# Kernel tuning notes

Measured on AMD Instinct MI355X. Metric: run time of the kernel, lower is better.

The kernel has to match this reference:

```python
import jax, jax.numpy as jnp
import numpy as np
import math

B, S, HID = 1, 2048, 4096
NH, NKV, HD = 32, 8, 128
N_REP = NH // NKV
ROPE_THETA = 10000.0


def setup_inputs() -> dict:
    key = jax.random.key(0)
    ks = jax.random.split(key, 5)
    hidden_states = jax.random.normal(ks[0], (B, S, HID), dtype=jnp.float32)
    # additive causal mask: 0 on/below diagonal, -1e9 above
    causal = jnp.triu(jnp.full((S, S), -1e9, dtype=jnp.float32), k=1)
    attention_mask = causal[None, None, :, :]
    wq = jax.random.normal(ks[1], (HID, NH * HD), dtype=jnp.float32) * 0.02
    wk = jax.random.normal(ks[2], (HID, NKV * HD), dtype=jnp.float32) * 0.02
    wv = jax.random.normal(ks[3], (HID, NKV * HD), dtype=jnp.float32) * 0.02
    wo = jax.random.normal(ks[4], (NH * HD, HID), dtype=jnp.float32) * 0.02
    return {"hidden_states": hidden_states, "attention_mask": attention_mask,
            "wq": wq, "wk": wk, "wv": wv, "wo": wo}


def _rope_cos_sin(seq_len, head_dim, base, dtype):
    inv_freq = 1.0 / (base ** (jnp.arange(0, head_dim, 2, dtype=jnp.float32) / head_dim))
    t = jnp.arange(seq_len, dtype=jnp.float32)
    freqs = jnp.outer(t, inv_freq)          # [S, HD/2]
    emb = jnp.concatenate([freqs, freqs], axis=-1)  # [S, HD]
    return jnp.cos(emb).astype(dtype), jnp.sin(emb).astype(dtype)


def _rotate_interleaved(x):
    # pairs (x0,x1) -> (-x1, x0), interleaved (matches torch stack/reshape trick)
    xp = x.reshape(*x.shape[:-1], -1, 2)
    return jnp.stack([-xp[..., 1], xp[..., 0]], axis=-1).reshape(x.shape)


def reference(hidden_states, attention_mask, wq, wk, wv, wo):
    b, s, _ = hidden_states.shape
    q = (hidden_states @ wq).reshape(b, s, NH, HD).transpose(0, 2, 1, 3)   # [B,NH,S,HD]
    k = (hidden_states @ wk).reshape(b, s, NKV, HD).transpose(0, 2, 1, 3)  # [B,NKV,S,HD]
    v = (hidden_states @ wv).reshape(b, s, NKV, HD).transpose(0, 2, 1, 3)

    cos, sin = _rope_cos_sin(s, HD, ROPE_THETA, hidden_states.dtype)
    cos = cos[None, None, :, :]  # broadcast over batch and heads
    sin = sin[None, None, :, :]
    q = q * cos + _rotate_interleaved(q) * sin
    k = k * cos + _rotate_interleaved(k) * sin

    # repeat_kv: [B,NKV,S,HD] -> [B,NH,S,HD]
    k = jnp.repeat(k, N_REP, axis=1)
    v = jnp.repeat(v, N_REP, axis=1)

    scores = jnp.einsum('bhqd,bhkd->bhqk', q, k) / math.sqrt(HD)
    scores = scores + attention_mask
    attn = jax.nn.softmax(scores.astype(jnp.float32), axis=-1).astype(q.dtype)
    out = jnp.einsum('bhqk,bhkd->bhqd', attn, v)          # [B,NH,S,HD]
    out = out.transpose(0, 2, 1, 3).reshape(b, s, NH * HD)
    return out @ wo
```

## Files before the change

### kernel.cpp

```cpp
#include <hip/hip_runtime.h>

#define S_LEN 2048
#define HID 4096
#define NH 32
#define NKV 8
#define HD 128
#define KVW 1024
#define NQKV 6144

typedef _Float16 f16;
typedef _Float16 f16x8 __attribute__((ext_vector_type(8)));
typedef _Float16 f16x4 __attribute__((ext_vector_type(4)));
typedef float f32x4 __attribute__((ext_vector_type(4)));
typedef float f32x16 __attribute__((ext_vector_type(16)));
typedef unsigned int u32;
typedef u32 u32x4 __attribute__((ext_vector_type(4)));

__device__ __forceinline__ void gll16(const void* g, void* lds) {
  __builtin_amdgcn_global_load_lds((const __attribute__((address_space(1))) void*)g,
                                   (__attribute__((address_space(3))) void*)lds, 16, 0, 0);
}

template<int N> __device__ __forceinline__ void vmwait() {
  if constexpr (N == 0) asm volatile("s_waitcnt vmcnt(0)" ::: "memory");
  else if constexpr (N == 3) asm volatile("s_waitcnt vmcnt(3)" ::: "memory");
  else if constexpr (N == 4) asm volatile("s_waitcnt vmcnt(4)" ::: "memory");
  else static_assert(N == 0 || N == 3 || N == 4, "add vmcnt case");
}

__global__ void k_cast(const float* __restrict__ src, f16* __restrict__ dst) {
  size_t i = ((size_t)blockIdx.x * blockDim.x + threadIdx.x) * 8;
  float4 a = *(const float4*)(src + i);
  float4 b = *(const float4*)(src + i + 4);
  f16x8 o = { (f16)a.x, (f16)a.y, (f16)a.z, (f16)a.w,
              (f16)b.x, (f16)b.y, (f16)b.z, (f16)b.w };
  *(f16x8*)(dst + i) = o;
}

__global__ void k_trig(float4* __restrict__ trig) {
  int id = blockIdx.x * blockDim.x + threadIdx.x;
  int s = id >> 6, i = id & 63;
  int j0 = 2 * i, j1 = 2 * i + 1;
  float f0 = powf(10000.f, -(float)(j0 & 63) / 64.f);
  float f1 = powf(10000.f, -(float)(j1 & 63) / 64.f);
  float a0 = (float)s * f0, a1 = (float)s * f1;
  trig[id] = make_float4(cosf(a0), cosf(a1), sinf(a0), sinf(a1));
}

__global__ void k_transpose(const float* __restrict__ src, f16* __restrict__ dst, int N) {
  __shared__ f16 tile[64][72];
  int nb = blockIdx.x * 64, kb = blockIdx.y * 64;
  int t = threadIdx.x;
  int kl = t >> 4, nc = (t & 15) << 2;
#pragma unroll
  for (int p = 0; p < 4; ++p) {
    int kk = kl + p * 16;
    float4 v = *(const float4*)(src + (size_t)(kb + kk) * N + nb + nc);
    f16x4 h = { (f16)v.x, (f16)v.y, (f16)v.z, (f16)v.w };
    *(f16x4*)(&tile[kk][nc]) = h;
  }
  __syncthreads();
  int nl = t >> 3, c = t & 7;
#pragma unroll
  for (int p = 0; p < 2; ++p) {
    int nn = nl + p * 32;
    f16x8 o;
#pragma unroll
    for (int i = 0; i < 8; ++i) o[i] = tile[c * 8 + i][nn];
    *(f16x8*)(dst + (size_t)(nb + nn) * HID + kb + c * 8) = o;
  }
}

extern __shared__ char smem[];

template<int MODE, int MF, int NF, int WM, int WN>
__global__ __launch_bounds__(WM * WN * 64, 2) void k_gemm4(
    const f16* __restrict__ A, const f16* __restrict__ Bt,
    f16* __restrict__ Qr, f16* __restrict__ Kr, f16* __restrict__ Vt,
    const float4* __restrict__ trig, float* __restrict__ Cout)
{
  constexpr int NTHR = WM * WN * 64;
  constexpr int BM = WM * MF * 16;
  constexpr int BN = WN * NF * 16;
  constexpr int ABYTES = BM * 128;
  constexpr int BBYTES = BN * 128;
  constexpr int RPC = NTHR / 8;
  constexpr int ACALLS = BM / RPC;
  constexpr int BCALLS = BN / RPC;
  constexpr int NT = 64;

  const int tid = threadIdx.x, ln = tid & 63, w = tid >> 6;
  const int la = ln & 15, lg = ln >> 4;
  const int wr = w / WN, wc = w % WN;
  const int m0 = blockIdx.y * BM, n0 = blockIdx.x * BN;

  const char* asrc[ACALLS];
  const char* bsrc[BCALLS];
  int adst[ACALLS > BCALLS ? ACALLS : BCALLS];
#pragma unroll
  for (int c = 0; c < ACALLS; ++c) {
    int r = c * RPC + (tid >> 3);
    int g = (tid & 7) ^ (r & 7);
    asrc[c] = (const char*)A + ((size_t)(m0 + r) * HID + (size_t)g * 8) * 2;
    adst[c] = c * NTHR * 16 + tid * 16;
  }
#pragma unroll
  for (int c = 0; c < BCALLS; ++c) {
    int r = c * RPC + (tid >> 3);
    int g = (tid & 7) ^ (r & 7);
    bsrc[c] = (const char*)Bt + ((size_t)(n0 + r) * HID + (size_t)g * 8) * 2;
  }

  char* const Bbase = smem + 2 * ABYTES;
  f32x4 acc[MF][NF] = {};

#pragma unroll
  for (int c = 0; c < ACALLS; ++c) gll16(asrc[c], smem + adst[c]);
#pragma unroll
  for (int c = 0; c < BCALLS; ++c) gll16(bsrc[c], Bbase + adst[c]);
#pragma unroll
  for (int c = 0; c < BCALLS; ++c) gll16(bsrc[c] + 128, Bbase + BBYTES + adst[c]);
  vmwait<BCALLS>();
  __builtin_amdgcn_s_barrier();

  for (int t = 0; t < NT; ++t) {
    if (t + 1 < NT) {
      char* sa = smem + ((t + 1) & 1) * ABYTES;
#pragma unroll
      for (int c = 0; c < ACALLS; ++c) gll16(asrc[c] + (size_t)(t + 1) * 128, sa + adst[c]);
    }
    if (t + 2 < NT) {
      char* sb = Bbase + ((t + 2) % 3) * BBYTES;
#pragma unroll
      for (int c = 0; c < BCALLS; ++c) gll16(bsrc[c] + (size_t)(t + 2) * 128, sb + adst[c]);
    }
    const char* sa = smem + (t & 1) * ABYTES;
    const char* sb = Bbase + (t % 3) * BBYTES;
#pragma unroll
    for (int ks = 0; ks < 2; ++ks) {
      f16x8 af[MF], bf[NF];
#pragma unroll
      for (int i = 0; i < MF; ++i) {
        int rl = wr * MF * 16 + i * 16 + la;
        af[i] = *(const f16x8*)(sa + rl * 128 + (((ks * 4 + lg) ^ (rl & 7)) * 16));
      }
#pragma unroll
      for (int n = 0; n < NF; ++n) {
        int rb = wc * NF * 16 + n * 16 + la;
        bf[n] = *(const f16x8*)(sb + rb * 128 + (((ks * 4 + lg) ^ (rb & 7)) * 16));
      }
#pragma unroll
      for (int i = 0; i < MF; ++i)
#pragma unroll
        for (int n = 0; n < NF; ++n)
          acc[i][n] = __builtin_amdgcn_mfma_f32_16x16x32_f16(af[i], bf[n], acc[i][n], 0, 0, 0);
    }
    if (t < NT - 2)      vmwait<BCALLS>();
    else if (t == NT - 2) vmwait<0>();
    if (t < NT - 1) __builtin_amdgcn_s_barrier();
  }

#pragma unroll
  for (int mi = 0; mi < MF; ++mi) {
#pragma unroll
    for (int nf = 0; nf < NF; ++nf) {
      f32x4 fr = acc[mi][nf];
      int n = n0 + wc * NF * 16 + nf * 16 + la;
      int mr = m0 + wr * MF * 16 + mi * 16 + lg * 4;
      if (MODE == 0) {
        if (n < HID + KVW) {
          int d = n & 127;
#pragma unroll
          for (int r = 0; r < 4; ++r) {
            float v = fr[r];
            float p = __shfl_xor(v, 1);
            float4 tc = trig[(size_t)(mr + r) * 64 + (d >> 1)];
            float cv = (d & 1) ? tc.y : tc.x;
            float sv = (d & 1) ? tc.w : tc.z;
            float o = v * cv + ((d & 1) ? p : -p) * sv;
            if (n < HID) Qr[(size_t)(mr + r) * HID + n] = (f16)o;
            else         Kr[(size_t)(mr + r) * KVW + (n - HID)] = (f16)o;
          }
        } else {
          int nv = n - (HID + KVW);
          f16x4 o4 = { (f16)fr[0], (f16)fr[1], (f16)fr[2], (f16)fr[3] };
          *(f16x4*)(Vt + (size_t)nv * S_LEN + mr) = o4;
        }
      } else {
#pragma unroll
        for (int r = 0; r < 4; ++r)
          Cout[(size_t)(mr + r) * HID + n] = fr[r];
      }
    }
  }
}

#define KBYTES (64 * 128 * 2)
#define VBYTES (128 * 64 * 2)

__global__ __launch_bounds__(256, 2) void k_attn(
    const f16* __restrict__ Qr, const f16* __restrict__ Kr, const f16* __restrict__ Vt,
    f16* __restrict__ AO)
{
  int bid = blockIdx.x;
  int h, c;
  if (bid < 256) { h = bid >> 3; c = bid & 7; }
  else           { int t = bid - 256; h = t >> 3; c = 15 - (t & 7); }
  const int hkv = h >> 2;
  const int q0c = c * 128;
  const int NT = 2 * c + 2;

  __shared__ char KV[2][KBYTES + VBYTES];

  const int tid = threadIdx.x;
  const int ln = tid & 63, w = tid >> 6;
  const int q = ln & 31;
  const int hi = ln >> 5;
  const int qg = q0c + w * 32 + q;

  size_t ksrc[4], vsrc[4];
  int kdo[4], vdo[4];
#pragma unroll
  for (int j = 0; j < 4; ++j) {
    int kc = w * 4 + j;
    int kr = kc * 4 + (ln >> 4);
    ksrc[j] = ((size_t)kr * KVW + hkv * HD) * 2 + (size_t)(((ln & 15) ^ (kr & 7)) * 16);
    kdo[j] = kc * 1024;
    int vc = w * 4 + j;
    int d = vc * 8 + (ln >> 3);
    vsrc[j] = ((size_t)(hkv * HD + d) * S_LEN) * 2 + (size_t)(((ln & 7) ^ (d & 7)) * 16);
    vdo[j] = KBYTES + vc * 1024;
  }

  f16x8 qf[8];
  {
    const f16* qrow = Qr + (size_t)qg * HID + h * HD + hi * 8;
#pragma unroll
    for (int ks = 0; ks < 8; ++ks) qf[ks] = *(const f16x8*)(qrow + ks * 16);
  }

  f32x16 ot[4] = {};
  float m2 = -3.0e38f, l = 0.f;
  const float K2 = 0.12753256471f;

  int buf = 0;
#pragma unroll
  for (int j = 0; j < 4; ++j) {
    gll16((const char*)Kr + ksrc[j], &KV[0][kdo[j]]);
    gll16((const char*)Vt + vsrc[j], &KV[0][vdo[j]]);
  }

  for (int jt = 0; jt < NT; ++jt) {
    __syncthreads();
    if (jt + 1 < NT) {
      size_t ko = (size_t)(jt + 1) * 64 * KVW * 2;
      size_t vo = (size_t)(jt + 1) * 64 * 2;
#pragma unroll
      for (int j = 0; j < 4; ++j) {
        gll16((const char*)Kr + ksrc[j] + ko, &KV[buf ^ 1][kdo[j]]);
        gll16((const char*)Vt + vsrc[j] + vo, &KV[buf ^ 1][vdo[j]]);
      }
    }
    const int j0 = jt * 64;
    if (j0 <= q0c + w * 32 + 31) {
      const f16* Kb = (const f16*)&KV[buf][0];
      const f16* Vb = (const f16*)&KV[buf][KBYTES];
      f32x16 s0 = {}, s1 = {};
#pragma unroll
      for (int ks = 0; ks < 8; ++ks) {
        int cc = ((ks * 2 + hi) ^ (q & 7)) * 8;
        f16x8 k0 = *(const f16x8*)(Kb + q * 128 + cc);
        f16x8 k1 = *(const f16x8*)(Kb + (q + 32) * 128 + cc);
        s0 = __builtin_amdgcn_mfma_f32_32x32x16_f16(k0, qf[ks], s0, 0, 0, 0);
        s1 = __builtin_amdgcn_mfma_f32_32x32x16_f16(k1, qf[ks], s1, 0, 0, 0);
      }
      const bool nm = (j0 + 63 > q0c + w * 32);
      float p0[16], p1[16];
      float mx = -3.0e38f;
#pragma unroll
      for (int r = 0; r < 16; ++r) {
        float a = s0[r], b = s1[r];
        if (nm) {
          int kvb = j0 + (r & 3) + 8 * (r >> 2) + 4 * hi;
          if (kvb > qg) a = -3.0e38f;
          if (kvb + 32 > qg) b = -3.0e38f;
        }
        p0[r] = a; p1[r] = b;
        mx = fmaxf(mx, fmaxf(a, b));
      }
      mx = fmaxf(mx, __shfl_xor(mx, 32));
      float m2c = mx * K2;
      int defer = (m2c <= m2 + 11.0f);
      if (!__all(defer)) {
        float m2n = fmaxf(m2, m2c);
        float corr = exp2f(m2 - m2n);
        m2 = m2n; l *= corr;
#pragma unroll
        for (int t = 0; t < 4; ++t)
#pragma unroll
          for (int r = 0; r < 16; ++r) ot[t][r] *= corr;
      }
      float sum = 0.f;
#pragma unroll
      for (int r = 0; r < 16; ++r) {
        p0[r] = exp2f(__builtin_fmaf(p0[r], K2, -m2));
        p1[r] = exp2f(__builtin_fmaf(p1[r], K2, -m2));
        sum += p0[r] + p1[r];
      }
      l += sum + __shfl_xor(sum, 32);
      u32 pw0[8], pw1[8];
#pragma unroll
      for (int t = 0; t < 8; ++t) {
        pw0[t] = __builtin_bit_cast(u32, __builtin_amdgcn_cvt_pkrtz(p0[2 * t], p0[2 * t + 1]));
        pw1[t] = __builtin_bit_cast(u32, __builtin_amdgcn_cvt_pkrtz(p1[2 * t], p1[2 * t + 1]));
      }
      f16x8 pf[4];
#pragma unroll
      for (int ch = 0; ch < 2; ++ch) {
        const u32* pw = ch ? pw1 : pw0;
        u32 sx[8];
#pragma unroll
        for (int t = 0; t < 8; ++t) sx[t] = (u32)__shfl_xor((int)pw[t], 32);
        u32x4 fa = { hi ? sx[2] : pw[0], hi ? sx[3] : pw[1],
                     hi ? pw[2] : sx[0], hi ? pw[3] : sx[1] };
        u32x4 fb = { hi ? sx[6] : pw[4], hi ? sx[7] : pw[5],
                     hi ? pw[6] : sx[4], hi ? pw[7] : sx[5] };
        pf[ch * 2 + 0] = __builtin_bit_cast(f16x8, fa);
        pf[ch * 2 + 1] = __builtin_bit_cast(f16x8, fb);
      }
#pragma unroll
      for (int dt = 0; dt < 4; ++dt) {
        int d = dt * 32 + q;
#pragma unroll
        for (int f = 0; f < 4; ++f) {
          f16x8 vf = *(const f16x8*)(Vb + d * 64 + (((f * 2 + hi) ^ (q & 7)) * 8));
          ot[dt] = __builtin_amdgcn_mfma_f32_32x32x16_f16(vf, pf[f], ot[dt], 0, 0, 0);
        }
      }
    }
    buf ^= 1;
  }

  __syncthreads();
  char* scr = &KV[0][0] + w * 8192;
  float inv = 1.f / l;
#pragma unroll
  for (int dt = 0; dt < 4; ++dt) {
#pragma unroll
    for (int rg = 0; rg < 4; ++rg) {
      u32 wa = __builtin_bit_cast(u32, __builtin_amdgcn_cvt_pkrtz(ot[dt][rg * 4 + 0] * inv, ot[dt][rg * 4 + 1] * inv));
      u32 wb = __builtin_bit_cast(u32, __builtin_amdgcn_cvt_pkrtz(ot[dt][rg * 4 + 2] * inv, ot[dt][rg * 4 + 3] * inv));
      int byte = q * 256 + (((dt * 4 + rg) ^ (q & 7)) * 16) + hi * 8;
      u32* p = (u32*)(scr + byte);
      p[0] = wa; p[1] = wb;
    }
  }
  asm volatile("s_waitcnt lgkmcnt(0)" ::: "memory");
#pragma unroll
  for (int ps = 0; ps < 8; ++ps) {
    int qr = ps * 4 + (ln >> 4);
    int ck = (ln & 15) ^ (qr & 7);
    f16x8 v = *(const f16x8*)(scr + qr * 256 + ck * 16);
    *(f16x8*)(AO + (size_t)(q0c + w * 32 + qr) * HID + h * HD + (ln & 15) * 8) = v;
  }
}

extern "C" void kernel_launch(void* const* d_in, const int* in_sizes, int n_in,
                              void* d_out, int out_size, void* d_ws, size_t ws_size,
                              hipStream_t stream) {
  const float* hs = (const float*)d_in[0];
  const float* wq = (const float*)d_in[2];
  const float* wk = (const float*)d_in[3];
  const float* wv = (const float*)d_in[4];
  const float* wo = (const float*)d_in[5];
  float* out = (float*)d_out;

  char* ws = (char*)d_ws;
  size_t off = 0;
  auto alloc = [&](size_t b) { char* p = ws + off; off += (b + 255) & ~(size_t)255; return p; };
  f16* Hh   = (f16*)alloc((size_t)S_LEN * HID * 2);
  f16* Wt   = (f16*)alloc((size_t)NQKV * HID * 2);
  float4* trig = (float4*)alloc((size_t)S_LEN * 64 * sizeof(float4));
  f16* Qrp  = (f16*)alloc((size_t)S_LEN * HID * 2);
  f16* Krp  = (f16*)alloc((size_t)S_LEN * KVW * 2);
  f16* Vtp  = (f16*)alloc((size_t)KVW * S_LEN * 2);
  f16* AO   = (f16*)alloc((size_t)S_LEN * HID * 2);
  f16* Wot  = (f16*)alloc((size_t)HID * HID * 2);

  hipFuncSetAttribute((const void*)k_gemm4<0, 8, 3, 2, 4>,
                      hipFuncAttributeMaxDynamicSharedMemorySize, 139264);
  hipFuncSetAttribute((const void*)k_gemm4<1, 4, 4, 2, 2>,
                      hipFuncAttributeMaxDynamicSharedMemorySize, 81920);

  k_cast<<<(S_LEN * HID) / (256 * 8), 256, 0, stream>>>(hs, Hh);
  k_trig<<<(S_LEN * 64) / 256, 256, 0, stream>>>(trig);
  k_transpose<<<dim3(HID / 64, HID / 64), 256, 0, stream>>>(wq, Wt, HID);
  k_transpose<<<dim3(KVW / 64, HID / 64), 256, 0, stream>>>(wk, Wt + (size_t)HID * HID, KVW);
  k_transpose<<<dim3(KVW / 64, HID / 64), 256, 0, stream>>>(wv, Wt + (size_t)(HID + KVW) * HID, KVW);
  k_transpose<<<dim3(HID / 64, HID / 64), 256, 0, stream>>>(wo, Wot, HID);
  k_gemm4<0, 8, 3, 2, 4><<<dim3(NQKV / 192, S_LEN / 256), 512, 139264, stream>>>(
      Hh, Wt, Qrp, Krp, Vtp, trig, nullptr);
  k_attn<<<dim3(512), 256, 0, stream>>>(Qrp, Krp, Vtp, AO);
  k_gemm4<1, 4, 4, 2, 2><<<dim3(HID / 128, S_LEN / 128), 256, 81920, stream>>>(
      AO, Wot, nullptr, nullptr, nullptr, nullptr, out);
}
```

Measured before the change: 340.1 us.

## Add 256x256 QKV GEMM with split-K LDS pipeline and merge weight transposes

Replaces the QKV projection GEMM with a new kernel using 256x256 tiles, a four-slot LDS ring split into k-halves, and fine-grained barrier-interleaved loads and MFMA phases with raised wave priority. The four weight transpose launches are merged into one kernel using 32x32 fp32 LDS tiles. s_setprio is also added around MFMA loops in the old GEMM. The goal is better data reuse per tile and overlap of global-to-LDS loads with compute. The cost is many extra barriers per k-step and a grid of only 24x8 blocks, which may underfill the device.

```diff
diff --git a/kernel.cpp b/kernel.cpp
--- a/kernel.cpp
+++ b/kernel.cpp
@@ -20,12 +20,13 @@
   __builtin_amdgcn_global_load_lds((const __attribute__((address_space(1))) void*)g,
                                    (__attribute__((address_space(3))) void*)lds, 16, 0, 0);
 }
+#define SFENCE asm volatile("" ::: "memory")
 
 template<int N> __device__ __forceinline__ void vmwait() {
   if constexpr (N == 0) asm volatile("s_waitcnt vmcnt(0)" ::: "memory");
-  else if constexpr (N == 3) asm volatile("s_waitcnt vmcnt(3)" ::: "memory");
   else if constexpr (N == 4) asm volatile("s_waitcnt vmcnt(4)" ::: "memory");
-  else static_assert(N == 0 || N == 3 || N == 4, "add vmcnt case");
+  else if constexpr (N == 6) asm volatile("s_waitcnt vmcnt(6)" ::: "memory");
+  else static_assert(N == 0 || N == 4 || N == 6, "add vmcnt case");
 }
 
 __global__ void k_cast(const float* __restrict__ src, f16* __restrict__ dst) {
@@ -47,31 +48,161 @@
   trig[id] = make_float4(cosf(a0), cosf(a1), sinf(a0), sinf(a1));
 }
 
-__global__ void k_transpose(const float* __restrict__ src, f16* __restrict__ dst, int N) {
-  __shared__ f16 tile[64][72];
-  int nb = blockIdx.x * 64, kb = blockIdx.y * 64;
+__global__ __launch_bounds__(256) void k_wprep(
+    const float* __restrict__ wq, const float* __restrict__ wk,
+    const float* __restrict__ wv, const float* __restrict__ wo,
+    f16* __restrict__ Wt, f16* __restrict__ Wot)
+{
+  __shared__ float tile[32][33];
+  int bid = blockIdx.x;
+  const float* src; f16* dst; int N; int r;
+  if (bid < 16384)      { src = wq; dst = Wt;                          N = 4096; r = bid; }
+  else if (bid < 20480) { src = wk; dst = Wt + (size_t)4096 * 4096;    N = 1024; r = bid - 16384; }
+  else if (bid < 24576) { src = wv; dst = Wt + (size_t)5120 * 4096;    N = 1024; r = bid - 20480; }
+  else                  { src = wo; dst = Wot;                         N = 4096; r = bid - 24576; }
+  int tpr = N >> 5;
+  int kb = (r / tpr) * 32, nb = (r % tpr) * 32;
   int t = threadIdx.x;
-  int kl = t >> 4, nc = (t & 15) << 2;
-#pragma unroll
-  for (int p = 0; p < 4; ++p) {
-    int kk = kl + p * 16;
-    float4 v = *(const float4*)(src + (size_t)(kb + kk) * N + nb + nc);
-    f16x4 h = { (f16)v.x, (f16)v.y, (f16)v.z, (f16)v.w };
-    *(f16x4*)(&tile[kk][nc]) = h;
+  {
+    int kl = t >> 3, ng = t & 7;
+    float4 v = *(const float4*)(src + (size_t)(kb + kl) * N + nb + ng * 4);
+    tile[kl][ng * 4 + 0] = v.x; tile[kl][ng * 4 + 1] = v.y;
+    tile[kl][ng * 4 + 2] = v.z; tile[kl][ng * 4 + 3] = v.w;
   }
   __syncthreads();
-  int nl = t >> 3, c = t & 7;
-#pragma unroll
-  for (int p = 0; p < 2; ++p) {
-    int nn = nl + p * 32;
-    f16x8 o;
-#pragma unroll
-    for (int i = 0; i < 8; ++i) o[i] = tile[c * 8 + i][nn];
-    *(f16x8*)(dst + (size_t)(nb + nn) * HID + kb + c * 8) = o;
+  {
+    int nl = t >> 3, kg = t & 7;
+    f16x4 o = { (f16)tile[kg * 4 + 0][nl], (f16)tile[kg * 4 + 1][nl],
+                (f16)tile[kg * 4 + 2][nl], (f16)tile[kg * 4 + 3][nl] };
+    *(f16x4*)(dst + (size_t)(nb + nl) * HID + kb + kg * 4) = o;
   }
 }
 
 extern __shared__ char smem[];
+
+__global__ __launch_bounds__(512, 2) void k_gemm5(
+    const f16* __restrict__ A, const f16* __restrict__ Bt,
+    f16* __restrict__ Qr, f16* __restrict__ Kr, f16* __restrict__ Vt,
+    const float4* __restrict__ trig)
+{
+  constexpr int NT = 64;
+  const int tid = threadIdx.x, ln = tid & 63, w = tid >> 6;
+  const int la = ln & 15, lg = ln >> 4;
+  const int wr = w >> 2, wc = w & 3;
+  const int m0 = blockIdx.y * 256, n0 = blockIdx.x * 256;
+
+  const char* asrc[2]; const char* bsrc[2];
+  {
+    int gr = ((tid & 3) ^ ((tid >> 4) & 3)) * 8;
+#pragma unroll
+    for (int g = 0; g < 2; ++g) {
+      int r = g * 128 + (tid >> 2);
+      asrc[g] = (const char*)A + ((size_t)(m0 + r) * HID + gr) * 2;
+      bsrc[g] = (const char*)Bt + ((size_t)(n0 + r) * HID + gr) * 2;
+    }
+  }
+  const int d16 = tid * 16;
+  auto stA = [&](int t, int kh) {
+    char* b = smem + (((2 * t + kh) & 3) * 16384) + d16;
+    size_t off = (size_t)t * 128 + kh * 64;
+    gll16(asrc[0] + off, b); gll16(asrc[1] + off, b + 8192);
+  };
+  auto stB = [&](int t, int kh) {
+    char* b = smem + 65536 + (((2 * t + kh) & 3) * 16384) + d16;
+    size_t off = (size_t)t * 128 + kh * 64;
+    gll16(bsrc[0] + off, b); gll16(bsrc[1] + off, b + 8192);
+  };
+  const int rcol = ((lg ^ (la >> 2)) & 3) * 16;
+  auto ldA = [&](f16x8* d, int t, int mh, int kh) {
+    const char* sb = smem + (((2 * t + kh) & 3) * 16384);
+#pragma unroll
+    for (int i = 0; i < 4; ++i) {
+      int rl = wr * 128 + mh * 64 + i * 16 + la;
+      d[i] = *(const f16x8*)(sb + rl * 64 + rcol);
+    }
+  };
+  auto ldB = [&](f16x8* d, int t, int kh) {
+    const char* sb = smem + 65536 + (((2 * t + kh) & 3) * 16384);
+#pragma unroll
+    for (int n = 0; n < 4; ++n) {
+      int rl = wc * 64 + n * 16 + la;
+      d[n] = *(const f16x8*)(sb + rl * 64 + rcol);
+    }
+  };
+
+  f32x4 acc[8][4] = {};
+  f16x8 af[4], bf[4];
+
+#define MM16(MH)                                                                     \
+  __builtin_amdgcn_s_setprio(1);                                                     \
+  _Pragma("unroll")                                                                  \
+  for (int i = 0; i < 4; ++i)                                                        \
+    _Pragma("unroll")                                                                \
+    for (int n = 0; n < 4; ++n)                                                      \
+      acc[(MH)*4 + i][n] =                                                           \
+        __builtin_amdgcn_mfma_f32_16x16x32_f16(af[i], bf[n], acc[(MH)*4 + i][n], 0, 0, 0); \
+  __builtin_amdgcn_s_setprio(0);
+
+#define LGKM0 asm volatile("s_waitcnt lgkmcnt(0)" ::: "memory")
+
+  stA(0, 0); stA(0, 1); stB(0, 0); stB(0, 1); stB(1, 0); stA(1, 0); stB(1, 1);
+  vmwait<6>(); __builtin_amdgcn_s_barrier();
+
+  for (int t = 0; t < NT; ++t) {
+    ldA(af, t, 0, 0); ldB(bf, t, 0);
+    if (t + 1 < NT) stA(t + 1, 1);
+    SFENCE; __builtin_amdgcn_s_barrier(); LGKM0;
+    MM16(0);
+    SFENCE; __builtin_amdgcn_s_barrier();
+    ldA(af, t, 1, 0);
+    if (t + 2 < NT) stB(t + 2, 0);
+    SFENCE; __builtin_amdgcn_s_barrier(); LGKM0;
+    MM16(1);
+    SFENCE; __builtin_amdgcn_s_barrier();
+    ldA(af, t, 0, 1); ldB(bf, t, 1);
+    if (t + 2 < NT) stA(t + 2, 0);
+    SFENCE; __builtin_amdgcn_s_barrier(); LGKM0;
+    MM16(0);
+    SFENCE; __builtin_amdgcn_s_barrier();
+    ldA(af, t, 1, 1);
+    if (t + 2 < NT) stB(t + 2, 1);
+    SFENCE; __builtin_amdgcn_s_barrier(); LGKM0;
+    MM16(1);
+    SFENCE;
+    if (t < NT - 2) vmwait<6>(); else vmwait<0>();
+    __builtin_amdgcn_s_barrier();
+  }
+#undef MM16
+#undef LGKM0
+
+#pragma unroll
+  for (int mi = 0; mi < 8; ++mi) {
+#pragma unroll
+    for (int nf = 0; nf < 4; ++nf) {
+      f32x4 fr = acc[mi][nf];
+      int n = n0 + wc * 64 + nf * 16 + la;
+      int mr = m0 + wr * 128 + mi * 16 + lg * 4;
+      if (n < HID + KVW) {
+        int d = n & 127;
+#pragma unroll
+        for (int r = 0; r < 4; ++r) {
+          float v = fr[r];
+          float p = __shfl_xor(v, 1);
+          float4 tc = trig[(size_t)(mr + r) * 64 + (d >> 1)];
+          float cv = (d & 1) ? tc.y : tc.x;
+          float sv = (d & 1) ? tc.w : tc.z;
+          float o = v * cv + ((d & 1) ? p : -p) * sv;
+          if (n < HID) Qr[(size_t)(mr + r) * HID + n] = (f16)o;
+          else         Kr[(size_t)(mr + r) * KVW + (n - HID)] = (f16)o;
+        }
+      } else {
+        int nv = n - (HID + KVW);
+        f16x4 o4 = { (f16)fr[0], (f16)fr[1], (f16)fr[2], (f16)fr[3] };
+        *(f16x4*)(Vt + (size_t)nv * S_LEN + mr) = o4;
+      }
+    }
+  }
+}
 
 template<int MODE, int MF, int NF, int WM, int WN>
 __global__ __launch_bounds__(WM * WN * 64, 2) void k_gemm4(
@@ -149,11 +280,13 @@
         int rb = wc * NF * 16 + n * 16 + la;
         bf[n] = *(const f16x8*)(sb + rb * 128 + (((ks * 4 + lg) ^ (rb & 7)) * 16));
       }
+      __builtin_amdgcn_s_setprio(1);
 #pragma unroll
       for (int i = 0; i < MF; ++i)
 #pragma unroll
         for (int n = 0; n < NF; ++n)
           acc[i][n] = __builtin_amdgcn_mfma_f32_16x16x32_f16(af[i], bf[n], acc[i][n], 0, 0, 0);
+      __builtin_amdgcn_s_setprio(0);
     }
     if (t < NT - 2)      vmwait<BCALLS>();
     else if (t == NT - 2) vmwait<0>();
@@ -168,24 +301,6 @@
       int n = n0 + wc * NF * 16 + nf * 16 + la;
       int mr = m0 + wr * MF * 16 + mi * 16 + lg * 4;
       if (MODE == 0) {
-        if (n < HID + KVW) {
-          int d = n & 127;
-#pragma unroll
-          for (int r = 0; r < 4; ++r) {
-            float v = fr[r];
-            float p = __shfl_xor(v, 1);
-            float4 tc = trig[(size_t)(mr + r) * 64 + (d >> 1)];
-            float cv = (d & 1) ? tc.y : tc.x;
-            float sv = (d & 1) ? tc.w : tc.z;
-            float o = v * cv + ((d & 1) ? p : -p) * sv;
-            if (n < HID) Qr[(size_t)(mr + r) * HID + n] = (f16)o;
-            else         Kr[(size_t)(mr + r) * KVW + (n - HID)] = (f16)o;
-          }
-        } else {
-          int nv = n - (HID + KVW);
-          f16x4 o4 = { (f16)fr[0], (f16)fr[1], (f16)fr[2], (f16)fr[3] };
-          *(f16x4*)(Vt + (size_t)nv * S_LEN + mr) = o4;
-        }
       } else {
 #pragma unroll
         for (int r = 0; r < 4; ++r)
@@ -387,19 +502,16 @@
   f16* AO   = (f16*)alloc((size_t)S_LEN * HID * 2);
   f16* Wot  = (f16*)alloc((size_t)HID * HID * 2);
 
-  hipFuncSetAttribute((const void*)k_gemm4<0, 8, 3, 2, 4>,
-                      hipFuncAttributeMaxDynamicSharedMemorySize, 139264);
+  hipFuncSetAttribute((const void*)k_gemm5,
+                      hipFuncAttributeMaxDynamicSharedMemorySize, 131072);
   hipFuncSetAttribute((const void*)k_gemm4<1, 4, 4, 2, 2>,
                       hipFuncAttributeMaxDynamicSharedMemorySize, 81920);
 
   k_cast<<<(S_LEN * HID) / (256 * 8), 256, 0, stream>>>(hs, Hh);
   k_trig<<<(S_LEN * 64) / 256, 256, 0, stream>>>(trig);
-  k_transpose<<<dim3(HID / 64, HID / 64), 256, 0, stream>>>(wq, Wt, HID);
-  k_transpose<<<dim3(KVW / 64, HID / 64), 256, 0, stream>>>(wk, Wt + (size_t)HID * HID, KVW);
-  k_transpose<<<dim3(KVW / 64, HID / 64), 256, 0, stream>>>(wv, Wt + (size_t)(HID + KVW) * HID, KVW);
-  k_transpose<<<dim3(HID / 64, HID / 64), 256, 0, stream>>>(wo, Wot, HID);
-  k_gemm4<0, 8, 3, 2, 4><<<dim3(NQKV / 192, S_LEN / 256), 512, 139264, stream>>>(
-      Hh, Wt, Qrp, Krp, Vtp, trig, nullptr);
+  k_wprep<<<40960, 256, 0, stream>>>(wq, wk, wv, wo, Wt, Wot);
+  k_gemm5<<<dim3(NQKV / 256, S_LEN / 256), 512, 131072, stream>>>(
+      Hh, Wt, Qrp, Krp, Vtp, trig);
   k_attn<<<dim3(512), 256, 0, stream>>>(Qrp, Krp, Vtp, AO);
   k_gemm4<1, 4, 4, 2, 2><<<dim3(HID / 128, S_LEN / 128), 256, 81920, stream>>>(
       AO, Wot, nullptr, nullptr, nullptr, nullptr, out);
```

After: 370.0 us. +8.8%, slower.
